# Kernel optimization log

Hardware: AMD Instinct MI355X
Metric: run time of the kernel (lower is better)

## Reference

```python
import jax, jax.numpy as jnp
import numpy as np
from jax import lax

N_QUBITS = 10
N_LAYERS = 6
DIM = 1 << N_QUBITS
EPS = 1e-5

_i = np.arange(DIM)
# Z_SIGNS[w, i] = (+1/-1) eigenvalue of PauliZ on wire w (wire 0 = most significant bit)
Z_SIGNS = jnp.asarray(np.stack([1.0 - 2.0 * ((_i >> (N_QUBITS - 1 - w)) & 1) for w in range(N_QUBITS)]).astype(np.float32))

def _layer_perm(r):
    # composed permutation of the ring of CNOT(w, (w+r)%n) gates of one StronglyEntanglingLayers layer
    p = _i.copy()
    for w in range(N_QUBITS):
        c, t = w, (w + r) % N_QUBITS
        pc, pt = N_QUBITS - 1 - c, N_QUBITS - 1 - t
        pg = _i ^ (((_i >> pc) & 1) << pt)
        p = p[pg]
    return p

LAYER_PERMS = [jnp.asarray(_layer_perm(l % (N_QUBITS - 1) + 1), dtype=jnp.int32) for l in range(N_LAYERS)]

def _apply_1q(state, U, wire):
    # state: (B, DIM) complex64; U: (2,2) or batched (B,2,2)
    B = state.shape[0]
    left = 1 << wire
    right = DIM // (2 * left)
    s = state.reshape(B, left, 2, right)
    if U.ndim == 3:
        out = jnp.einsum('bij,bljr->blir', U, s)
    else:
        out = jnp.einsum('ij,bljr->blir', U, s)
    return out.reshape(B, DIM)

def _ry_batched(theta):
    c = jnp.cos(theta / 2)
    s = jnp.sin(theta / 2)
    return jnp.stack([jnp.stack([c, -s], -1), jnp.stack([s, c], -1)], -2).astype(jnp.complex64)

def _rot(phi, theta, omega):
    # PennyLane Rot(phi, theta, omega) = RZ(omega) @ RY(theta) @ RZ(phi)
    c = jnp.cos(theta / 2)
    s = jnp.sin(theta / 2)
    m00 = jnp.exp(-1j * (phi + omega) / 2) * c
    m01 = -jnp.exp(1j * (phi - omega) / 2) * s
    m10 = jnp.exp(-1j * (phi - omega) / 2) * s
    m11 = jnp.exp(1j * (phi + omega) / 2) * c
    return jnp.stack([jnp.stack([m00, m01]), jnp.stack([m10, m11])]).astype(jnp.complex64)

def quantum_forward(xq, qw):
    # batched statevector simulation of: RY(pi*x_i) encoding + StronglyEntanglingLayers
    B = xq.shape[0]
    state = jnp.zeros((B, DIM), jnp.complex64).at[:, 0].set(1.0)
    for w in range(N_QUBITS):
        state = _apply_1q(state, _ry_batched(jnp.pi * xq[:, w]), w)
    for l in range(N_LAYERS):
        for w in range(N_QUBITS):
            state = _apply_1q(state, _rot(qw[l, w, 0], qw[l, w, 1], qw[l, w, 2]), w)
        state = state[:, LAYER_PERMS[l]]
    probs = state.real ** 2 + state.imag ** 2
    return probs @ Z_SIGNS.T  # (B, N_QUBITS) expvals of PauliZ

def _conv(x, w, b):
    y = lax.conv_general_dilated(x, w, (1, 1), 'SAME', dimension_numbers=('NCHW', 'OIHW', 'NCHW'))
    return y + b[None, :, None, None]

def _bn(x, g, b):
    # BatchNorm2d in training mode: per-batch statistics over (N, H, W)
    m = jnp.mean(x, (0, 2, 3), keepdims=True)
    v = jnp.var(x, (0, 2, 3), keepdims=True)
    return (x - m) * lax.rsqrt(v + EPS) * g[None, :, None, None] + b[None, :, None, None]

def _pool(x):
    return lax.reduce_window(x, -jnp.inf, lax.max, (1, 1, 2, 2), (1, 1, 2, 2), 'VALID')

def setup_inputs() -> dict:
    key = jax.random.key(0)
    ks = jax.random.split(key, 16)
    n = lambda k, sh, sc: jax.random.normal(k, sh, jnp.float32) * sc
    return {
        'x': jax.random.normal(ks[0], (256, 3, 64, 64), jnp.float32),
        'conv1_w': n(ks[1], (32, 3, 3, 3), 0.1), 'conv1_b': jnp.zeros(32),
        'bn1_g': jnp.ones(32), 'bn1_b': jnp.zeros(32),
        'conv2_w': n(ks[2], (32, 32, 3, 3), 0.05), 'conv2_b': jnp.zeros(32),
        'bn2_g': jnp.ones(32), 'bn2_b': jnp.zeros(32),
        'conv3_w': n(ks[3], (64, 32, 3, 3), 0.05), 'conv3_b': jnp.zeros(64),
        'bn3_g': jnp.ones(64), 'bn3_b': jnp.zeros(64),
        'conv4_w': n(ks[4], (64, 64, 3, 3), 0.05), 'conv4_b': jnp.zeros(64),
        'bn4_g': jnp.ones(64), 'bn4_b': jnp.zeros(64),
        'fc1_w': n(ks[5], (128, 64 * 16 * 16), 0.01), 'fc1_b': jnp.zeros(128),
        'fc2_w': n(ks[6], (10, 128), 0.05), 'fc2_b': jnp.zeros(10),
        'q_weights': jax.random.uniform(ks[7], (6, 10, 3), jnp.float32),
        'head_w': n(ks[8], (10, 10), 0.1), 'head_b': jnp.zeros(10),
    }

def reference(x, conv1_w, conv1_b, bn1_g, bn1_b, conv2_w, conv2_b, bn2_g, bn2_b,
              conv3_w, conv3_b, bn3_g, bn3_b, conv4_w, conv4_b, bn4_g, bn4_b,
              fc1_w, fc1_b, fc2_w, fc2_b, q_weights, head_w, head_b):
    h = jax.nn.relu(_bn(_conv(x, conv1_w, conv1_b), bn1_g, bn1_b))
    h = jax.nn.relu(_bn(_conv(h, conv2_w, conv2_b), bn2_g, bn2_b))
    h = _pool(h)  # Dropout(0.25) is identity in eval
    h = jax.nn.relu(_bn(_conv(h, conv3_w, conv3_b), bn3_g, bn3_b))
    h = jax.nn.relu(_bn(_conv(h, conv4_w, conv4_b), bn4_g, bn4_b))
    h = _pool(h)
    h = h.reshape(h.shape[0], -1)  # (B, 64*16*16)
    h = jax.nn.relu(h @ fc1_w.T + fc1_b)
    h = h @ fc2_w.T + fc2_b  # (B, n_qubits)
    q = quantum_forward(h, q_weights)
    return q @ head_w.T + head_b  # (B, num_classes)
```

## Files before the change

### kernel.cpp

```cpp
#include <hip/hip_runtime.h>
#include <math.h>

#define PI_F 3.14159265358979323846f

typedef __attribute__((ext_vector_type(8))) _Float16 half8;
typedef __attribute__((ext_vector_type(4))) _Float16 half4;
typedef __attribute__((ext_vector_type(4))) float f32x4;

__global__ __launch_bounds__(256) void prep_kernel(
    const float* __restrict__ x, _Float16* __restrict__ X4P,
    const float* __restrict__ w1, const float* __restrict__ w2,
    const float* __restrict__ w3, const float* __restrict__ w4,
    _Float16* __restrict__ t1, _Float16* __restrict__ t2,
    _Float16* __restrict__ t3, _Float16* __restrict__ t4,
    const float* __restrict__ f1w, _Float16* __restrict__ w1t,
    const float* __restrict__ qw, float* __restrict__ rotm,
    unsigned short* __restrict__ perm)
{
    const int b = blockIdx.x;
    const int t = threadIdx.x;
    if (b < 2380) {
        int pp = (b * 256 + t) * 2;
        half8 o;
        #pragma unroll
        for (int j = 0; j < 2; ++j) {
            int p = pp + j;
            int n = p / 4760;
            int rem = p - n * 4760;
            int yp = rem / 68, xp = rem - (rem / 68) * 68;
            int gy = yp - 2, gx = xp - 2;
            float v0 = 0.f, v1 = 0.f, v2 = 0.f;
            if (gy >= 0 && gy < 64 && gx >= 0 && gx < 64) {
                const float* xb = x + (size_t)n * 12288 + gy * 64 + gx;
                v0 = xb[0]; v1 = xb[4096]; v2 = xb[8192];
            }
            o[j * 4 + 0] = (_Float16)v0;
            o[j * 4 + 1] = (_Float16)v1;
            o[j * 4 + 2] = (_Float16)v2;
            o[j * 4 + 3] = (_Float16)0.f;
        }
        *(half8*)&X4P[(size_t)pp * 4] = o;
    } else if (b < 2640) {
        int idx = (b - 2380) * 256 + t;
        if (idx < 9216) {
            int j = idx & 7, co = (idx >> 3) & 31, k8 = idx >> 8;
            int k = k8 * 8 + j, tap = k >> 5, ci = k & 31;
            t2[idx] = (_Float16)w2[(size_t)(co * 32 + ci) * 9 + tap];
        } else if (idx < 27648) {
            int e = idx - 9216;
            int j = e & 7, co = (e >> 3) & 31, r = e >> 8;
            int k8 = r % 36, gg = r / 36;
            int k = k8 * 8 + j, tap = k >> 5, ci = k & 31;
            t3[e] = (_Float16)w3[(size_t)((gg * 32 + co) * 32 + ci) * 9 + tap];
        } else if (idx < 64512) {
            int e = idx - 27648;
            int j = e & 7, co = (e >> 3) & 31, r = e >> 8;
            int k8 = r % 36, gc = r / 36;
            int g = gc >> 1, cc = gc & 1;
            int kl = k8 * 8 + j, tap = kl >> 5, ci = cc * 32 + (kl & 31);
            t4[e] = (_Float16)w4[(size_t)((g * 32 + co) * 64 + ci) * 9 + tap];
        } else if (idx < 66560) {
            int e = idx - 64512;
            int j = e & 7, co = (e >> 3) & 31, k8 = e >> 8;
            int k = k8 * 8 + j, tap = k >> 2, ci = k & 3;
            t1[e] = (_Float16)((tap < 9 && ci < 3) ? w1[(size_t)(co * 3 + ci) * 9 + tap] : 0.f);
        }
    } else if (b < 3152) {
        __shared__ float lds[64][65];
        int b2 = b - 2640;
        const int yx0 = (b2 & 3) * 64;
        const int j = b2 >> 2;
        #pragma unroll
        for (int i = 0; i < 16; ++i) {
            int idx = t + 256 * i;
            int c = idx >> 6, yxl = idx & 63;
            lds[c][yxl] = f1w[(size_t)j * 16384 + c * 256 + yx0 + yxl];
        }
        __syncthreads();
        #pragma unroll
        for (int i = 0; i < 2; ++i) {
            int idx = t + 256 * i;
            int yxl = idx >> 3, c8 = idx & 7;
            half8 h;
            #pragma unroll
            for (int jj = 0; jj < 8; ++jj)
                h[jj] = (_Float16)lds[c8 * 8 + jj][yxl];
            *(half8*)&w1t[(size_t)j * 16384 + (size_t)(yx0 + yxl) * 64 + c8 * 8] = h;
        }
    } else {
        if (t < 60) {
            float phi = qw[t * 3], th = qw[t * 3 + 1], om = qw[t * 3 + 2];
            float c = cosf(0.5f * th), s = sinf(0.5f * th);
            float apo = 0.5f * (phi + om), amo = 0.5f * (phi - om);
            float cpo = cosf(apo), spo = sinf(apo);
            float cmo = cosf(amo), smo = sinf(amo);
            rotm[t * 8 + 0] = cpo * c;  rotm[t * 8 + 1] = -spo * c;
            rotm[t * 8 + 2] = -cmo * s; rotm[t * 8 + 3] = -smo * s;
            rotm[t * 8 + 4] = cmo * s;  rotm[t * 8 + 5] = -smo * s;
            rotm[t * 8 + 6] = cpo * c;  rotm[t * 8 + 7] = spo * c;
        }
        for (int e = t; e < 6144; e += 256) {
            int layer = e >> 10, i = e & 1023;
            int r = layer % 9 + 1;
            int jdx = i;
            for (int w = 9; w >= 0; --w) {
                int tt = (w + r) % 10;
                int pc = 9 - w, pt_ = 9 - tt;
                jdx ^= ((jdx >> pc) & 1) << pt_;
            }
            perm[e] = (unsigned short)jdx;
        }
    }
}

__global__ __launch_bounds__(256) void conv1_stats_kernel(
    const _Float16* __restrict__ X4P, const _Float16* __restrict__ w1m,
    const float* __restrict__ bias, float* __restrict__ partials)
{
    constexpr int TC = 66, TR = 6;
    constexpr int NPIX = (TR + 1) * TC;
    __shared__ __align__(16) _Float16 s_in[NPIX * 4];
    __shared__ __align__(16) _Float16 s_w[2048];
    __shared__ float s_red[64];

    const int t = threadIdx.x;
    const int row0 = blockIdx.x * 4;
    const int n = blockIdx.z;

    *(half8*)&s_w[t * 8] = *(const half8*)&w1m[t * 8];

    for (int p = t; p < NPIX; p += 256) {
        int col = p % TC, r = p / TC;
        uint2 u = make_uint2(0u, 0u);
        if (r < TR) {
            size_t pb = ((size_t)(n * 70 + row0 + r + 1) * 68 + col + 1) * 4;
            u = *(const uint2*)&X4P[pb];
        }
        *(uint2*)&s_in[p * 4] = u;
    }
    if (t < 64) s_red[t] = 0.f;
    __syncthreads();

    const int w = t >> 6, l = t & 63;
    const int lm = l & 15, lg = l >> 4;
    int pA[4];
    #pragma unroll
    for (int f = 0; f < 4; ++f) {
        int m = w * 64 + f * 16 + lm;
        pA[f] = (m >> 6) * TC + (m & 63);
    }
    f32x4 zero4 = {0.f, 0.f, 0.f, 0.f};
    f32x4 acc[4][2];
    #pragma unroll
    for (int f = 0; f < 4; ++f) { acc[f][0] = zero4; acc[f][1] = zero4; }

    {
        const int t0 = lg * 2;
        const int off0 = (t0 / 3) * TC + (t0 % 3);
        const int off1 = ((t0 + 1) / 3) * TC + ((t0 + 1) % 3);
        half8 b0 = *(const half8*)&s_w[(lg * 32 + lm) * 8];
        half8 b1 = *(const half8*)&s_w[(lg * 32 + 16 + lm) * 8];
        #pragma unroll
        for (int f = 0; f < 4; ++f) {
            half4 alo = *(const half4*)&s_in[(pA[f] + off0) * 4];
            half4 ahi = *(const half4*)&s_in[(pA[f] + off1) * 4];
            half8 a;
            #pragma unroll
            for (int j = 0; j < 4; ++j) { a[j] = alo[j]; a[4 + j] = ahi[j]; }
            acc[f][0] = __builtin_amdgcn_mfma_f32_16x16x32_f16(a, b0, acc[f][0], 0, 0, 0);
            acc[f][1] = __builtin_amdgcn_mfma_f32_16x16x32_f16(a, b1, acc[f][1], 0, 0, 0);
        }
    }
    {
        half8 b0 = *(const half8*)&s_w[((4 + lg) * 32 + lm) * 8];
        half8 b1 = *(const half8*)&s_w[((4 + lg) * 32 + 16 + lm) * 8];
        #pragma unroll
        for (int f = 0; f < 4; ++f) {
            half8 a;
            #pragma unroll
            for (int j = 0; j < 8; ++j) a[j] = (_Float16)0.f;
            if (lg == 0) {
                half4 alo = *(const half4*)&s_in[(pA[f] + 134) * 4];
                half4 ahi = *(const half4*)&s_in[(pA[f] + 198) * 4];
                #pragma unroll
                for (int j = 0; j < 4; ++j) { a[j] = alo[j]; a[4 + j] = ahi[j]; }
            }
            acc[f][0] = __builtin_amdgcn_mfma_f32_16x16x32_f16(a, b0, acc[f][0], 0, 0, 0);
            acc[f][1] = __builtin_amdgcn_mfma_f32_16x16x32_f16(a, b1, acc[f][1], 0, 0, 0);
        }
    }

    float bv0 = bias[lm];
    float bv1 = bias[16 + lm];
    float s0 = 0.f, s20 = 0.f, s1 = 0.f, s21 = 0.f;
    #pragma unroll
    for (int f = 0; f < 4; ++f) {
        #pragma unroll
        for (int r = 0; r < 4; ++r) {
            float v0 = acc[f][0][r] + bv0;
            float v1 = acc[f][1][r] + bv1;
            s0 += v0; s20 += v0 * v0;
            s1 += v1; s21 += v1 * v1;
        }
    }
    s0 += __shfl_xor(s0, 16);  s0 += __shfl_xor(s0, 32);
    s1 += __shfl_xor(s1, 16);  s1 += __shfl_xor(s1, 32);
    s20 += __shfl_xor(s20, 16); s20 += __shfl_xor(s20, 32);
    s21 += __shfl_xor(s21, 16); s21 += __shfl_xor(s21, 32);
    if (l < 16) {
        atomicAdd(&s_red[lm], s0);
        atomicAdd(&s_red[16 + lm], s1);
        atomicAdd(&s_red[32 + lm], s20);
        atomicAdd(&s_red[48 + lm], s21);
    }
    __syncthreads();
    if (t < 64)
        partials[((size_t)n * 16 + blockIdx.x) * 64 + t] = s_red[t];
}

__global__ __launch_bounds__(512, 6) void conv2_fused_kernel(
    const _Float16* __restrict__ X4P, const _Float16* __restrict__ w1m,
    const float* __restrict__ c1bias, const _Float16* __restrict__ ssh1,
    const _Float16* __restrict__ wt2, const float* __restrict__ c2bias,
    _Float16* __restrict__ out0, _Float16* __restrict__ out1,
    float* __restrict__ partials)
{
    constexpr int COUT = 32, MF = 4, NB = 2;
    constexpr int ROWS = 8;
    constexpr int TC = 66, NPIX = 10 * 66;
    constexpr int PS = 36;
    constexpr int XC = 68;
    __shared__ __align__(16) _Float16 s_in[NPIX * PS];
    __shared__ __align__(16) _Float16 s_w1[2048];
    __shared__ float s_red[64];

    const int t = threadIdx.x;
    const int row0 = blockIdx.x * ROWS;
    const int n = blockIdx.z;
    const int w = t >> 6, l = t & 63;
    const int lm = l & 15, lg = l >> 4;

    const _Float16* Xb = X4P + ((size_t)(n * 70 + row0) * 68) * 4;

    if (t < 256) *(half8*)&s_w1[t * 8] = *(const half8*)&w1m[t * 8];
    if (t < 64) s_red[t] = 0.f;
    __syncthreads();

    {
        const float b1v0 = c1bias[lm], b1v1 = c1bias[16 + lm];
        const _Float16 sc0 = ssh1[lm], sh0 = ssh1[32 + lm];
        const _Float16 sc1 = ssh1[16 + lm], sh1 = ssh1[48 + lm];
        for (int g = w; g < 42; g += 8) {
            int py = g * 16 + lm;
            int pyc = py < NPIX ? py : 0;
            int ry = pyc / 66, cy = pyc - ry * 66;
            int pb = ry * XC + cy;
            f32x4 a0 = {0.f, 0.f, 0.f, 0.f}, a1 = {0.f, 0.f, 0.f, 0.f};
            {
                const int t0 = lg * 2;
                const int off0 = (t0 / 3) * XC + (t0 % 3);
                const int off1 = ((t0 + 1) / 3) * XC + ((t0 + 1) % 3);
                half8 b0 = *(const half8*)&s_w1[(lg * 32 + lm) * 8];
                half8 b1 = *(const half8*)&s_w1[(lg * 32 + 16 + lm) * 8];
                half4 alo = *(const half4*)&Xb[(size_t)(pb + off0) * 4];
                half4 ahi = *(const half4*)&Xb[(size_t)(pb + off1) * 4];
                half8 a;
                #pragma unroll
                for (int j = 0; j < 4; ++j) { a[j] = alo[j]; a[4 + j] = ahi[j]; }
                a0 = __builtin_amdgcn_mfma_f32_16x16x32_f16(a, b0, a0, 0, 0, 0);
                a1 = __builtin_amdgcn_mfma_f32_16x16x32_f16(a, b1, a1, 0, 0, 0);
            }
            {
                half8 b0 = *(const half8*)&s_w1[((4 + lg) * 32 + lm) * 8];
                half8 b1 = *(const half8*)&s_w1[((4 + lg) * 32 + 16 + lm) * 8];
                half8 a;
                #pragma unroll
                for (int j = 0; j < 8; ++j) a[j] = (_Float16)0.f;
                if (lg == 0) {
                    half4 alo = *(const half4*)&Xb[(size_t)(pb + 138) * 4];
                    half4 ahi = *(const half4*)&Xb[(size_t)(pb + 204) * 4];
                    #pragma unroll
                    for (int j = 0; j < 4; ++j) { a[j] = alo[j]; a[4 + j] = ahi[j]; }
                }
                a0 = __builtin_amdgcn_mfma_f32_16x16x32_f16(a, b0, a0, 0, 0, 0);
                a1 = __builtin_amdgcn_mfma_f32_16x16x32_f16(a, b1, a1, 0, 0, 0);
            }
            #pragma unroll
            for (int r2 = 0; r2 < 4; ++r2) {
                int py2 = g * 16 + lg * 4 + r2;
                if (py2 < NPIX) {
                    int r2y = py2 / 66, c2y = py2 - r2y * 66;
                    int gy = row0 - 1 + r2y, gx = c2y - 1;
                    _Float16 y0 = (_Float16)0.f, y1 = (_Float16)0.f;
                    if (gy >= 0 && gy < 64 && gx >= 0 && gx < 64) {
                        _Float16 v0 = (_Float16)(a0[r2] + b1v0);
                        _Float16 v1 = (_Float16)(a1[r2] + b1v1);
                        _Float16 f0 = v0 * sc0 + sh0;
                        _Float16 f1 = v1 * sc1 + sh1;
                        y0 = f0 > (_Float16)0.f ? f0 : (_Float16)0.f;
                        y1 = f1 > (_Float16)0.f ? f1 : (_Float16)0.f;
                    }
                    s_in[py2 * PS + lm] = y0;
                    s_in[py2 * PS + 16 + lm] = y1;
                }
            }
        }
    }
    __syncthreads();

    int pA[MF];
    #pragma unroll
    for (int f = 0; f < MF; ++f)
        pA[f] = w * TC + f * 16 + lm;
    f32x4 zero4 = {0.f, 0.f, 0.f, 0.f};
    f32x4 acc[MF][NB];
    #pragma unroll
    for (int f = 0; f < MF; ++f)
        #pragma unroll
        for (int nb = 0; nb < NB; ++nb) acc[f][nb] = zero4;

    #pragma unroll
    for (int tap = 0; tap < 9; ++tap) {
        const int dy = tap / 3, dx = tap % 3;
        const int poff = dy * TC + dx;
        half8 b[NB];
        #pragma unroll
        for (int nb = 0; nb < NB; ++nb) {
            int col = nb * 16 + lm;
            b[nb] = *(const half8*)&wt2[((tap * 4 + lg) * 32 + col) * 8];
        }
        #pragma unroll
        for (int f = 0; f < MF; ++f) {
            int p = pA[f] + poff;
            half4 alo = *(const half4*)&s_in[p * PS + lg * 8];
            half4 ahi = *(const half4*)&s_in[p * PS + lg * 8 + 4];
            half8 a;
            #pragma unroll
            for (int j = 0; j < 4; ++j) { a[j] = alo[j]; a[4 + j] = ahi[j]; }
            #pragma unroll
            for (int nb = 0; nb < NB; ++nb)
                acc[f][nb] = __builtin_amdgcn_mfma_f32_16x16x32_f16(a, b[nb], acc[f][nb], 0, 0, 0);
        }
    }

    float bv[NB], s[NB], s2[NB];
    #pragma unroll
    for (int nb = 0; nb < NB; ++nb) {
        bv[nb] = c2bias[nb * 16 + lm];
        s[nb] = 0.f; s2[nb] = 0.f;
    }
    #pragma unroll
    for (int f = 0; f < MF; ++f) {
        #pragma unroll
        for (int nb = 0; nb < NB; ++nb) {
            #pragma unroll
            for (int r = 0; r < 4; ++r) {
                float v = acc[f][nb][r] + bv[nb];
                acc[f][nb][r] = v;
                s[nb] += v; s2[nb] += v * v;
            }
        }
    }
    #pragma unroll
    for (int nb = 0; nb < NB; ++nb) {
        s[nb] += __shfl_xor(s[nb], 16);  s[nb] += __shfl_xor(s[nb], 32);
        s2[nb] += __shfl_xor(s2[nb], 16); s2[nb] += __shfl_xor(s2[nb], 32);
    }
    if (l < 16) {
        #pragma unroll
        for (int nb = 0; nb < NB; ++nb) {
            atomicAdd(&s_red[nb * 16 + lm], s[nb]);
            atomicAdd(&s_red[32 + nb * 16 + lm], s2[nb]);
        }
    }

    {
        __syncthreads();
        _Float16* pk = s_in;
        #pragma unroll
        for (int nb = 0; nb < NB; ++nb) {
            #pragma unroll
            for (int f = 0; f < MF; ++f) {
                float v0 = acc[f][nb][0], v1 = acc[f][nb][1];
                float v2 = acc[f][nb][2], v3 = acc[f][nb][3];
                int xp0 = f * 8 + lg * 2;
                int o0 = (w * 32 + xp0) * COUT + nb * 16 + lm;
                int o1 = (w * 32 + xp0 + 1) * COUT + nb * 16 + lm;
                pk[o0] = (_Float16)fminf(v0, v1);
                pk[8192 + o0] = (_Float16)fmaxf(v0, v1);
                pk[o1] = (_Float16)fminf(v2, v3);
                pk[8192 + o1] = (_Float16)fmaxf(v2, v3);
            }
        }
        __syncthreads();
        int hp_row = t >> 7, rem = t & 127;
        int xp = rem >> 2, c8 = rem & 3;
        half8 mnA = *(const half8*)&pk[((2 * hp_row) * 32 + xp) * COUT + c8 * 8];
        half8 mnB = *(const half8*)&pk[((2 * hp_row + 1) * 32 + xp) * COUT + c8 * 8];
        half8 mxA = *(const half8*)&pk[8192 + ((2 * hp_row) * 32 + xp) * COUT + c8 * 8];
        half8 mxB = *(const half8*)&pk[8192 + ((2 * hp_row + 1) * 32 + xp) * COUT + c8 * 8];
        half8 mn, mx;
        #pragma unroll
        for (int j = 0; j < 8; ++j) {
            mn[j] = mnA[j] < mnB[j] ? mnA[j] : mnB[j];
            mx[j] = mxA[j] > mxB[j] ? mxA[j] : mxB[j];
        }
        size_t ob = (((size_t)n * 32 + (row0 >> 1) + hp_row) * 32 + xp) * COUT + c8 * 8;
        *(half8*)&out0[ob] = mn;
        *(half8*)&out1[ob] = mx;
    }

    __syncthreads();
    if (t < 64) {
        size_t bid = (size_t)n * gridDim.x + blockIdx.x;
        partials[bid * 64 + t] = s_red[t];
    }
}

template<int BLOCK, int W, int CIN, int COUT, int MF, int NB,
         bool MMIN, bool POOL>
__global__ __launch_bounds__(BLOCK, (BLOCK == 512 ? 4 : 3)) void conv_mfma_kernel(
    const _Float16* __restrict__ in0, const _Float16* __restrict__ in1,
    const _Float16* __restrict__ coef, const _Float16* __restrict__ wt,
    const float* __restrict__ bias,
    _Float16* __restrict__ out0, _Float16* __restrict__ out1,
    float* __restrict__ partials)
{
    constexpr int H = W;
    constexpr int NWAVE = BLOCK / 64;
    constexpr int SPW = MF * 16;
    constexpr int ROWS = NWAVE * SPW / W;
    constexpr int TR = ROWS + 2;
    constexpr int TC = W + 2;
    constexpr int NPIX = TR * TC;
    constexpr int NCH = CIN / 32;
    constexpr int C8N = CIN / 8;
    constexpr int KC = 288;
    constexpr int COUTB = NB * 16;
    __shared__ __align__(16) _Float16 s_in[NPIX * CIN];
    __shared__ float s_red[2 * COUTB];

    const int t = threadIdx.x;
    const int row0 = blockIdx.x * ROWS;
    const int n = blockIdx.z;

    const int w = t >> 6, l = t & 63;
    const int lm = l & 15, lg = l >> 4;
    int pA[MF];
    #pragma unroll
    for (int f = 0; f < MF; ++f) {
        int m = w * SPW + f * 16 + lm;
        pA[f] = (m / W) * TC + (m % W);
    }
    f32x4 zero4 = {0.f, 0.f, 0.f, 0.f};
    f32x4 acc[MF][NB];
    #pragma unroll
    for (int f = 0; f < MF; ++f)
        #pragma unroll
        for (int nb = 0; nb < NB; ++nb) acc[f][nb] = zero4;
    if (t < 2 * COUTB) s_red[t] = 0.f;

    for (int idx = t; idx < NPIX * C8N; idx += BLOCK) {
        int c8 = idx % C8N;
        int p = idx / C8N;
        int col = p % TC, r = p / TC;
        int gy = row0 + r - 1, gx = col - 1;
        half8 v;
        #pragma unroll
        for (int j = 0; j < 8; ++j) v[j] = (_Float16)0.f;
        if (gy >= 0 && gy < H && gx >= 0 && gx < W) {
            size_t gidx = (((size_t)n * H + gy) * W + gx) * CIN + c8 * 8;
            if (MMIN) {
                half8 mn = *(const half8*)&in0[gidx];
                half8 mx = *(const half8*)&in1[gidx];
                half8 sa = *(const half8*)&coef[c8 * 8];
                half8 sb = *(const half8*)&coef[CIN + c8 * 8];
                half8 sh = *(const half8*)&coef[2 * CIN + c8 * 8];
                #pragma unroll
                for (int j = 0; j < 8; ++j) {
                    _Float16 f = mx[j] * sa[j] + mn[j] * sb[j] + sh[j];
                    v[j] = f > (_Float16)0.f ? f : (_Float16)0.f;
                }
            } else {
                v = *(const half8*)&in0[gidx];
                if (coef) {
                    half8 sc = *(const half8*)&coef[c8 * 8];
                    half8 sh = *(const half8*)&coef[CIN + c8 * 8];
                    #pragma unroll
                    for (int j = 0; j < 8; ++j) {
                        _Float16 f = v[j] * sc[j] + sh[j];
                        v[j] = f > (_Float16)0.f ? f : (_Float16)0.f;
                    }
                }
            }
        }
        *(half8*)&s_in[(c8 * NPIX + p) * 8] = v;
    }
    __syncthreads();

    #pragma unroll
    for (int tap = 0; tap < 9; ++tap) {
        const int dy = tap / 3, dx = tap % 3;
        const int poff = dy * TC + dx;
        #pragma unroll
        for (int cc = 0; cc < NCH; ++cc) {
            half8 b[NB];
            #pragma unroll
            for (int nb = 0; nb < NB; ++nb) {
                int cog = nb * 16 + lm;
                int gg = cog >> 5, col = cog & 31;
                const _Float16* wp = wt + (size_t)(gg * NCH + cc) * KC * 32;
                b[nb] = *(const half8*)&wp[((tap * 4 + lg) * 32 + col) * 8];
            }
            #pragma unroll
            for (int f = 0; f < MF; ++f) {
                half8 a = *(const half8*)&s_in[((cc * 4 + lg) * NPIX + pA[f] + poff) * 8];
                #pragma unroll
                for (int nb = 0; nb < NB; ++nb)
                    acc[f][nb] = __builtin_amdgcn_mfma_f32_16x16x32_f16(a, b[nb], acc[f][nb], 0, 0, 0);
            }
        }
    }

    float bv[NB], s[NB], s2[NB];
    #pragma unroll
    for (int nb = 0; nb < NB; ++nb) {
        bv[nb] = bias[nb * 16 + lm];
        s[nb] = 0.f; s2[nb] = 0.f;
    }
    #pragma unroll
    for (int f = 0; f < MF; ++f) {
        #pragma unroll
        for (int r = 0; r < 4; ++r) {
            int m = w * SPW + f * 16 + lg * 4 + r;
            int yy = row0 + m / W, xo = m % W;
            size_t base = (((size_t)n * H + yy) * W + xo) * COUT;
            #pragma unroll
            for (int nb = 0; nb < NB; ++nb) {
                float v = acc[f][nb][r] + bv[nb];
                if (!POOL) out0[base + nb * 16 + lm] = (_Float16)v;
                s[nb] += v; s2[nb] += v * v;
            }
        }
    }
    #pragma unroll
    for (int nb = 0; nb < NB; ++nb) {
        s[nb] += __shfl_xor(s[nb], 16);  s[nb] += __shfl_xor(s[nb], 32);
        s2[nb] += __shfl_xor(s2[nb], 16); s2[nb] += __shfl_xor(s2[nb], 32);
    }
    if (l < 16) {
        #pragma unroll
        for (int nb = 0; nb < NB; ++nb) {
            atomicAdd(&s_red[nb * 16 + lm], s[nb]);
            atomicAdd(&s_red[COUTB + nb * 16 + lm], s2[nb]);
        }
    }

    if (POOL) {
        constexpr int FH = MF / 2;
        constexpr int PPIX = (ROWS / 2) * (W / 2);
        static_assert(2 * PPIX * COUT <= NPIX * CIN, "pool pack fits in s_in");
        __syncthreads();
        _Float16* pk = s_in;
        #pragma unroll
        for (int nb = 0; nb < NB; ++nb) {
            #pragma unroll
            for (int f = 0; f < FH; ++f) {
                #pragma unroll
                for (int rp = 0; rp < 2; ++rp) {
                    float a0 = acc[f][nb][2 * rp] + bv[nb];
                    float a1 = acc[f][nb][2 * rp + 1] + bv[nb];
                    float a2 = acc[f + FH][nb][2 * rp] + bv[nb];
                    float a3 = acc[f + FH][nb][2 * rp + 1] + bv[nb];
                    float mn = fminf(fminf(a0, a1), fminf(a2, a3));
                    float mx = fmaxf(fmaxf(a0, a1), fmaxf(a2, a3));
                    int xp = f * 8 + lg * 2 + rp;
                    int o = (w * (W / 2) + xp) * COUT + nb * 16 + lm;
                    pk[o] = (_Float16)mn;
                    pk[PPIX * COUT + o] = (_Float16)mx;
                }
            }
        }
        __syncthreads();
        size_t gb = (((size_t)n * (H / 2) + (row0 >> 1)) * (W / 2)) * COUT;
        for (int idx = t; idx < PPIX * COUT / 8; idx += BLOCK) {
            *(half8*)&out0[gb + (size_t)idx * 8] = *(const half8*)&pk[idx * 8];
            *(half8*)&out1[gb + (size_t)idx * 8] = *(const half8*)&pk[(PPIX * COUT + idx * 8)];
        }
    }

    __syncthreads();
    if (t < 2 * COUTB) {
        size_t bid = (size_t)n * gridDim.x + blockIdx.x;
        partials[bid * 2 * COUTB + t] = s_red[t];
    }
}

__global__ __launch_bounds__(256) void bn_finalize_kernel(
    const float* __restrict__ partials, int nx, float inv_count,
    const float* __restrict__ gamma, const float* __restrict__ beta,
    float* __restrict__ ss, _Float16* __restrict__ ssh,
    _Float16* __restrict__ sab, int COUT)
{
    const int c = blockIdx.x;
    const int t = threadIdx.x;
    float sum = 0.f, sq = 0.f;
    int total = 256 * nx;
    for (int e = t; e < total; e += 256) {
        size_t off = (size_t)e * 2 * COUT;
        sum += partials[off + c];
        sq  += partials[off + COUT + c];
    }
    #pragma unroll
    for (int off = 32; off > 0; off >>= 1) {
        sum += __shfl_xor(sum, off);
        sq  += __shfl_xor(sq, off);
    }
    __shared__ float rs[4], rq[4];
    if ((t & 63) == 0) { rs[t >> 6] = sum; rq[t >> 6] = sq; }
    __syncthreads();
    if (t == 0) {
        sum = rs[0] + rs[1] + rs[2] + rs[3];
        sq  = rq[0] + rq[1] + rq[2] + rq[3];
        float mean = sum * inv_count;
        float var = sq * inv_count - mean * mean;
        float scale = gamma[c] * rsqrtf(var + 1e-5f);
        float shift = beta[c] - mean * scale;
        ss[c] = scale;
        ss[COUT + c] = shift;
        if (ssh) {
            ssh[c] = (_Float16)scale;
            ssh[COUT + c] = (_Float16)shift;
        }
        if (sab) {
            sab[c] = (_Float16)(scale > 0.f ? scale : 0.f);
            sab[COUT + c] = (_Float16)(scale > 0.f ? 0.f : scale);
            sab[2 * COUT + c] = (_Float16)shift;
        }
    }
}

__global__ __launch_bounds__(256) void fc1_mfma_kernel(
    const _Float16* __restrict__ Amin, const _Float16* __restrict__ Amax,
    const _Float16* __restrict__ sab, const _Float16* __restrict__ Bw,
    float* __restrict__ hp)
{
    __shared__ __align__(16) _Float16 As[64][72];
    __shared__ __align__(16) _Float16 Bs[128][72];
    const int t = threadIdx.x;
    const int mt = blockIdx.x;
    const int kc = blockIdx.y;
    const int w = t >> 6, l = t & 63;
    const int lm = l & 15, lg = l >> 4;

    f32x4 zero4 = {0.f, 0.f, 0.f, 0.f};
    f32x4 acc[8];
    #pragma unroll
    for (int nb = 0; nb < 8; ++nb) acc[nb] = zero4;

    const size_t a_base = (size_t)(mt * 64) * 16384 + (size_t)kc * 512;
    const size_t b_base = (size_t)kc * 512;

    for (int p = 0; p < 8; ++p) {
        __syncthreads();
        #pragma unroll
        for (int i = 0; i < 2; ++i) {
            int idx = t + 256 * i;
            int r = idx >> 3, c8 = idx & 7;
            size_t off = a_base + (size_t)r * 16384 + p * 64 + c8 * 8;
            half8 mn = *(const half8*)&Amin[off];
            half8 mx = *(const half8*)&Amax[off];
            half8 sa = *(const half8*)&sab[c8 * 8];
            half8 sb = *(const half8*)&sab[64 + c8 * 8];
            half8 sh = *(const half8*)&sab[128 + c8 * 8];
            half8 v;
            #pragma unroll
            for (int j = 0; j < 8; ++j) {
                _Float16 f = mx[j] * sa[j] + mn[j] * sb[j] + sh[j];
                v[j] = f > (_Float16)0.f ? f : (_Float16)0.f;
            }
            *(half8*)&As[r][c8 * 8] = v;
        }
        #pragma unroll
        for (int i = 0; i < 4; ++i) {
            int idx = t + 256 * i;
            int r = idx >> 3, c8 = idx & 7;
            *(half8*)&Bs[r][c8 * 8] =
                *(const half8*)&Bw[b_base + (size_t)r * 16384 + p * 64 + c8 * 8];
        }
        __syncthreads();
        #pragma unroll
        for (int ks = 0; ks < 64; ks += 32) {
            half8 a = *(const half8*)&As[w * 16 + lm][ks + lg * 8];
            #pragma unroll
            for (int nb = 0; nb < 8; ++nb) {
                half8 b = *(const half8*)&Bs[nb * 16 + lm][ks + lg * 8];
                acc[nb] = __builtin_amdgcn_mfma_f32_16x16x32_f16(a, b, acc[nb], 0, 0, 0);
            }
        }
    }
    #pragma unroll
    for (int nb = 0; nb < 8; ++nb) {
        #pragma unroll
        for (int r = 0; r < 4; ++r) {
            int row = mt * 64 + w * 16 + lg * 4 + r;
            hp[((size_t)kc * 256 + row) * 128 + nb * 16 + lm] = acc[nb][r];
        }
    }
}

__global__ __launch_bounds__(128) void fcq_kernel(
    const float* __restrict__ hp, const float* __restrict__ f1b,
    const float* __restrict__ f2w, const float* __restrict__ f2b,
    const float* __restrict__ rotm, const unsigned short* __restrict__ perm,
    const float* __restrict__ head_w, const float* __restrict__ head_b,
    float* __restrict__ outp)
{
    __shared__ float lds[2048];
    __shared__ float hl[128];
    __shared__ float xql[10];
    const int n = blockIdx.x;
    const int t = threadIdx.x;

    {
        float s = f1b[t];
        #pragma unroll
        for (int kc = 0; kc < 32; ++kc) s += hp[((size_t)kc * 256 + n) * 128 + t];
        hl[t] = fmaxf(0.f, s);
    }
    __syncthreads();
    if (t < 10) {
        float o = f2b[t];
        #pragma unroll 4
        for (int k = 0; k < 128; ++k) o += f2w[t * 128 + k] * hl[k];
        xql[t] = o;
    }
    __syncthreads();
    if (t >= 64) return;

    const int l = t;
    float ar[16], ai[16];
    #pragma unroll
    for (int r = 0; r < 16; ++r) { ar[r] = 0.f; ai[r] = 0.f; }
    if (l == 0) ar[0] = 1.f;

    #pragma unroll
    for (int w = 0; w < 10; ++w) {
        float th = 0.5f * PI_F * xql[w];
        float c = cosf(th), s = sinf(th);
        const int k = 9 - w;
        if (k >= 6) {
            const int b = k - 6;
            #pragma unroll
            for (int r = 0; r < 16; ++r) {
                if (!(r & (1 << b))) {
                    int r1 = r | (1 << b);
                    float a0 = ar[r], a1 = ar[r1];
                    ar[r]  = c * a0 - s * a1;
                    ar[r1] = s * a0 + c * a1;
                }
            }
        } else {
            float ss = ((l >> k) & 1) ? s : -s;
            #pragma unroll
            for (int r = 0; r < 16; ++r) {
                float p = __shfl_xor(ar[r], 1 << k);
                ar[r] = c * ar[r] + ss * p;
            }
        }
    }

    #pragma unroll 1
    for (int layer = 0; layer < 6; ++layer) {
        #pragma unroll
        for (int w = 0; w < 10; ++w) {
            const float* m = rotm + (layer * 10 + w) * 8;
            float m00r = m[0], m00i = m[1], m01r = m[2], m01i = m[3];
            float m10r = m[4], m10i = m[5], m11r = m[6], m11i = m[7];
            const int k = 9 - w;
            if (k >= 6) {
                const int b = k - 6;
                #pragma unroll
                for (int r = 0; r < 16; ++r) {
                    if (!(r & (1 << b))) {
                        int r1 = r | (1 << b);
                        float a0r = ar[r], a0i = ai[r];
                        float a1r = ar[r1], a1i = ai[r1];
                        ar[r]  = m00r * a0r - m00i * a0i + m01r * a1r - m01i * a1i;
                        ai[r]  = m00r * a0i + m00i * a0r + m01r * a1i + m01i * a1r;
                        ar[r1] = m10r * a0r - m10i * a0i + m11r * a1r - m11i * a1i;
                        ai[r1] = m10r * a0i + m10i * a0r + m11r * a1i + m11i * a1r;
                    }
                }
            } else {
                int bit = (l >> k) & 1;
                float mAr = bit ? m11r : m00r, mAi = bit ? m11i : m00i;
                float mBr = bit ? m10r : m01r, mBi = bit ? m10i : m01i;
                #pragma unroll
                for (int r = 0; r < 16; ++r) {
                    float pr = __shfl_xor(ar[r], 1 << k);
                    float pi = __shfl_xor(ai[r], 1 << k);
                    float mr = ar[r], mi = ai[r];
                    ar[r] = mAr * mr - mAi * mi + mBr * pr - mBi * pi;
                    ai[r] = mAr * mi + mAi * mr + mBr * pi + mBi * pr;
                }
            }
        }
        #pragma unroll
        for (int r = 0; r < 16; ++r) {
            lds[(r << 6) | l] = ar[r];
            lds[1024 + ((r << 6) | l)] = ai[r];
        }
        __syncthreads();
        const unsigned short* pt = perm + layer * 1024;
        #pragma unroll
        for (int r = 0; r < 16; ++r) {
            int ji = pt[(r << 6) | l];
            ar[r] = lds[ji];
            ai[r] = lds[1024 + ji];
        }
        __syncthreads();
    }

    float S = 0.f, T0 = 0.f, T1 = 0.f, T2 = 0.f, T3 = 0.f;
    #pragma unroll
    for (int r = 0; r < 16; ++r) {
        float pr = ar[r] * ar[r] + ai[r] * ai[r];
        S += pr;
        T0 += (r & 1) ? -pr : pr;
        T1 += (r & 2) ? -pr : pr;
        T2 += (r & 4) ? -pr : pr;
        T3 += (r & 8) ? -pr : pr;
    }
    float pk[10];
    pk[0] = T3; pk[1] = T2; pk[2] = T1; pk[3] = T0;
    #pragma unroll
    for (int w = 4; w < 10; ++w)
        pk[w] = ((l >> (9 - w)) & 1) ? -S : S;
    #pragma unroll
    for (int w = 0; w < 10; ++w) {
        #pragma unroll
        for (int off = 1; off < 64; off <<= 1)
            pk[w] += __shfl_xor(pk[w], off);
    }
    if (l < 10) {
        float o = head_b[l];
        #pragma unroll
        for (int kk = 0; kk < 10; ++kk) o += pk[kk] * head_w[l * 10 + kk];
        outp[n * 10 + l] = o;
    }
}

extern "C" void kernel_launch(void* const* d_in, const int* in_sizes, int n_in,
                              void* d_out, int out_size, void* d_ws, size_t ws_size,
                              hipStream_t stream)
{
    const float* x   = (const float*)d_in[0];
    const float* c1w = (const float*)d_in[1];  const float* c1b = (const float*)d_in[2];
    const float* g1  = (const float*)d_in[3];  const float* b1  = (const float*)d_in[4];
    const float* c2w = (const float*)d_in[5];  const float* c2b = (const float*)d_in[6];
    const float* g2  = (const float*)d_in[7];  const float* b2  = (const float*)d_in[8];
    const float* c3w = (const float*)d_in[9];  const float* c3b = (const float*)d_in[10];
    const float* g3  = (const float*)d_in[11]; const float* b3  = (const float*)d_in[12];
    const float* c4w = (const float*)d_in[13]; const float* c4b = (const float*)d_in[14];
    const float* g4  = (const float*)d_in[15]; const float* b4  = (const float*)d_in[16];
    const float* f1w = (const float*)d_in[17]; const float* f1b = (const float*)d_in[18];
    const float* f2w = (const float*)d_in[19]; const float* f2b = (const float*)d_in[20];
    const float* qw  = (const float*)d_in[21];
    const float* hw  = (const float*)d_in[22]; const float* hb  = (const float*)d_in[23];

    float* ws = (float*)d_ws;
    _Float16* H0 = (_Float16*)ws;
    _Float16* H1 = H0 + 33554432;
    float* part = ws + 33554432;
    float* ss1  = part + 524288;
    float* ss2  = ss1 + 64;
    float* ss3  = ss2 + 64;
    float* ss4  = ss3 + 128;
    float* hp   = ss4 + 128;
    float* rotm = hp + 1048576;
    unsigned short* perm16 = (unsigned short*)(rotm + 480);
    _Float16* ssh1 = (_Float16*)(perm16 + 6144);
    _Float16* ssh3 = ssh1 + 64;
    _Float16* sab2 = ssh3 + 128;
    _Float16* sab4 = sab2 + 96;
    _Float16* wt2  = sab4 + 192;
    _Float16* wt3  = wt2 + 9216;
    _Float16* wt4  = wt3 + 18432;
    _Float16* w1m  = wt4 + 36864;
    _Float16* w1t  = w1m + 2048;
    _Float16* X4P  = w1t + 2097152;

    _Float16* minT2 = H1;
    _Float16* maxT2 = H1 + 8388608;
    _Float16* minT4 = H1;
    _Float16* maxT4 = H1 + 4194304;

    prep_kernel<<<3153, 256, 0, stream>>>(x, X4P, c1w, c2w, c3w, c4w,
                                          w1m, wt2, wt3, wt4, f1w, w1t,
                                          qw, rotm, perm16);

    conv1_stats_kernel<<<dim3(16, 1, 256), 256, 0, stream>>>(X4P, w1m, c1b, part);
    bn_finalize_kernel<<<32, 256, 0, stream>>>(part, 16, 1.f / 1048576.f,
                                               g1, b1, ss1, ssh1, nullptr, 32);

    conv2_fused_kernel<<<dim3(8, 1, 256), 512, 0, stream>>>(
        X4P, w1m, c1b, ssh1, wt2, c2b, minT2, maxT2, part);
    bn_finalize_kernel<<<32, 256, 0, stream>>>(part, 8, 1.f / 1048576.f,
                                               g2, b2, ss2, nullptr, sab2, 32);

    conv_mfma_kernel<512, 32, 32, 64, 4, 4, true, false>
        <<<dim3(2, 1, 256), 512, 0, stream>>>(
        minT2, maxT2, sab2, wt3, c3b, H0, nullptr, part);
    bn_finalize_kernel<<<64, 256, 0, stream>>>(part, 2, 1.f / 262144.f,
                                               g3, b3, ss3, ssh3, nullptr, 64);

    conv_mfma_kernel<512, 32, 64, 64, 4, 4, false, true>
        <<<dim3(2, 1, 256), 512, 0, stream>>>(
        H0, nullptr, ssh3, wt4, c4b, minT4, maxT4, part);
    bn_finalize_kernel<<<64, 256, 0, stream>>>(part, 2, 1.f / 262144.f,
                                               g4, b4, ss4, nullptr, sab4, 64);

    fc1_mfma_kernel<<<dim3(4, 32), 256, 0, stream>>>(minT4, maxT4, sab4, w1t, hp);

    fcq_kernel<<<256, 128, 0, stream>>>(hp, f1b, f2w, f2b,
                                        rotm, perm16, hw, hb, (float*)d_out);
}
```

Measured before the change: 194.0 us.

## Materialize conv1 output in fp16 instead of recomputing it inside conv2

```diff
diff --git a/kernel.cpp b/kernel.cpp
--- a/kernel.cpp
+++ b/kernel.cpp
@@ -115,12 +115,14 @@
 
 __global__ __launch_bounds__(256) void conv1_stats_kernel(
     const _Float16* __restrict__ X4P, const _Float16* __restrict__ w1m,
-    const float* __restrict__ bias, float* __restrict__ partials)
+    const float* __restrict__ bias, _Float16* __restrict__ Yg,
+    float* __restrict__ partials)
 {
     constexpr int TC = 66, TR = 6;
     constexpr int NPIX = (TR + 1) * TC;
     __shared__ __align__(16) _Float16 s_in[NPIX * 4];
     __shared__ __align__(16) _Float16 s_w[2048];
+    __shared__ __align__(16) _Float16 s_y[256 * 32];
     __shared__ float s_red[64];
 
     const int t = threadIdx.x;
@@ -199,6 +201,9 @@
         for (int r = 0; r < 4; ++r) {
             float v0 = acc[f][0][r] + bv0;
             float v1 = acc[f][1][r] + bv1;
+            int p_loc = w * 64 + f * 16 + lg * 4 + r;
+            s_y[p_loc * 32 + lm] = (_Float16)v0;
+            s_y[p_loc * 32 + 16 + lm] = (_Float16)v1;
             s0 += v0; s20 += v0 * v0;
             s1 += v1; s21 += v1 * v1;
         }
@@ -214,13 +219,21 @@
         atomicAdd(&s_red[48 + lm], s21);
     }
     __syncthreads();
+
+    {
+        _Float16* Yb = Yg + ((size_t)(n * 64 + row0) * 64) * 32;
+        #pragma unroll
+        for (int i = 0; i < 4; ++i) {
+            int idx = t + 256 * i;
+            *(half8*)&Yb[(size_t)idx * 8] = *(const half8*)&s_y[idx * 8];
+        }
+    }
     if (t < 64)
         partials[((size_t)n * 16 + blockIdx.x) * 64 + t] = s_red[t];
 }
 
 __global__ __launch_bounds__(512, 6) void conv2_fused_kernel(
-    const _Float16* __restrict__ X4P, const _Float16* __restrict__ w1m,
-    const float* __restrict__ c1bias, const _Float16* __restrict__ ssh1,
+    const _Float16* __restrict__ Yg, const _Float16* __restrict__ ssh1,
     const _Float16* __restrict__ wt2, const float* __restrict__ c2bias,
     _Float16* __restrict__ out0, _Float16* __restrict__ out1,
     float* __restrict__ partials)
@@ -229,9 +242,7 @@
     constexpr int ROWS = 8;
     constexpr int TC = 66, NPIX = 10 * 66;
     constexpr int PS = 36;
-    constexpr int XC = 68;
     __shared__ __align__(16) _Float16 s_in[NPIX * PS];
-    __shared__ __align__(16) _Float16 s_w1[2048];
     __shared__ float s_red[64];
 
     const int t = threadIdx.x;
@@ -240,70 +251,30 @@
     const int w = t >> 6, l = t & 63;
     const int lm = l & 15, lg = l >> 4;
 
-    const _Float16* Xb = X4P + ((size_t)(n * 70 + row0) * 68) * 4;
-
-    if (t < 256) *(half8*)&s_w1[t * 8] = *(const half8*)&w1m[t * 8];
     if (t < 64) s_red[t] = 0.f;
-    __syncthreads();
 
     {
-        const float b1v0 = c1bias[lm], b1v1 = c1bias[16 + lm];
-        const _Float16 sc0 = ssh1[lm], sh0 = ssh1[32 + lm];
-        const _Float16 sc1 = ssh1[16 + lm], sh1 = ssh1[48 + lm];
-        for (int g = w; g < 42; g += 8) {
-            int py = g * 16 + lm;
-            int pyc = py < NPIX ? py : 0;
-            int ry = pyc / 66, cy = pyc - ry * 66;
-            int pb = ry * XC + cy;
-            f32x4 a0 = {0.f, 0.f, 0.f, 0.f}, a1 = {0.f, 0.f, 0.f, 0.f};
-            {
-                const int t0 = lg * 2;
-                const int off0 = (t0 / 3) * XC + (t0 % 3);
-                const int off1 = ((t0 + 1) / 3) * XC + ((t0 + 1) % 3);
-                half8 b0 = *(const half8*)&s_w1[(lg * 32 + lm) * 8];
-                half8 b1 = *(const half8*)&s_w1[(lg * 32 + 16 + lm) * 8];
-                half4 alo = *(const half4*)&Xb[(size_t)(pb + off0) * 4];
-                half4 ahi = *(const half4*)&Xb[(size_t)(pb + off1) * 4];
-                half8 a;
+        const int c8 = t & 3;
+        half8 sc = *(const half8*)&ssh1[c8 * 8];
+        half8 sh = *(const half8*)&ssh1[32 + c8 * 8];
+        for (int idx = t; idx < NPIX * 4; idx += 512) {
+            int p = idx >> 2;
+            int py = p / 66, px = p - py * 66;
+            int gy = row0 - 1 + py, gx = px - 1;
+            half8 v;
+            #pragma unroll
+            for (int j = 0; j < 8; ++j) v[j] = (_Float16)0.f;
+            if (gy >= 0 && gy < 64 && gx >= 0 && gx < 64) {
+                half8 y = *(const half8*)&Yg[(((size_t)n * 64 + gy) * 64 + gx) * 32 + c8 * 8];
                 #pragma unroll
-                for (int j = 0; j < 4; ++j) { a[j] = alo[j]; a[4 + j] = ahi[j]; }
-                a0 = __builtin_amdgcn_mfma_f32_16x16x32_f16(a, b0, a0, 0, 0, 0);
-                a1 = __builtin_amdgcn_mfma_f32_16x16x32_f16(a, b1, a1, 0, 0, 0);
-            }
-            {
-                half8 b0 = *(const half8*)&s_w1[((4 + lg) * 32 + lm) * 8];
-                half8 b1 = *(const half8*)&s_w1[((4 + lg) * 32 + 16 + lm) * 8];
-                half8 a;
-                #pragma unroll
-                for (int j = 0; j < 8; ++j) a[j] = (_Float16)0.f;
-                if (lg == 0) {
-                    half4 alo = *(const half4*)&Xb[(size_t)(pb + 138) * 4];
-                    half4 ahi = *(const half4*)&Xb[(size_t)(pb + 204) * 4];
-                    #pragma unroll
-                    for (int j = 0; j < 4; ++j) { a[j] = alo[j]; a[4 + j] = ahi[j]; }
+                for (int j = 0; j < 8; ++j) {
+                    _Float16 f = y[j] * sc[j] + sh[j];
+                    v[j] = f > (_Float16)0.f ? f : (_Float16)0.f;
                 }
-                a0 = __builtin_amdgcn_mfma_f32_16x16x32_f16(a, b0, a0, 0, 0, 0);
-                a1 = __builtin_amdgcn_mfma_f32_16x16x32_f16(a, b1, a1, 0, 0, 0);
-            }
-            #pragma unroll
-            for (int r2 = 0; r2 < 4; ++r2) {
-                int py2 = g * 16 + lg * 4 + r2;
-                if (py2 < NPIX) {
-                    int r2y = py2 / 66, c2y = py2 - r2y * 66;
-                    int gy = row0 - 1 + r2y, gx = c2y - 1;
-                    _Float16 y0 = (_Float16)0.f, y1 = (_Float16)0.f;
-                    if (gy >= 0 && gy < 64 && gx >= 0 && gx < 64) {
-                        _Float16 v0 = (_Float16)(a0[r2] + b1v0);
-                        _Float16 v1 = (_Float16)(a1[r2] + b1v1);
-                        _Float16 f0 = v0 * sc0 + sh0;
-                        _Float16 f1 = v1 * sc1 + sh1;
-                        y0 = f0 > (_Float16)0.f ? f0 : (_Float16)0.f;
-                        y1 = f1 > (_Float16)0.f ? f1 : (_Float16)0.f;
-                    }
-                    s_in[py2 * PS + lm] = y0;
-                    s_in[py2 * PS + 16 + lm] = y1;
-                }
-            }
+            }
+            half4* vp = (half4*)&v;
+            *(half4*)&s_in[p * PS + c8 * 8] = vp[0];
+            *(half4*)&s_in[p * PS + c8 * 8 + 4] = vp[1];
         }
     }
     __syncthreads();
@@ -891,6 +862,7 @@
     _Float16* w1t  = w1m + 2048;
     _Float16* X4P  = w1t + 2097152;
 
+    _Float16* Yg    = H0;
     _Float16* minT2 = H1;
     _Float16* maxT2 = H1 + 8388608;
     _Float16* minT4 = H1;
@@ -900,12 +872,13 @@
                                           w1m, wt2, wt3, wt4, f1w, w1t,
                                           qw, rotm, perm16);
 
-    conv1_stats_kernel<<<dim3(16, 1, 256), 256, 0, stream>>>(X4P, w1m, c1b, part);
+    conv1_stats_kernel<<<dim3(16, 1, 256), 256, 0, stream>>>(
+        X4P, w1m, c1b, Yg, part);
     bn_finalize_kernel<<<32, 256, 0, stream>>>(part, 16, 1.f / 1048576.f,
                                                g1, b1, ss1, ssh1, nullptr, 32);
 
     conv2_fused_kernel<<<dim3(8, 1, 256), 512, 0, stream>>>(
-        X4P, w1m, c1b, ssh1, wt2, c2b, minT2, maxT2, part);
+        Yg, ssh1, wt2, c2b, minT2, maxT2, part);
     bn_finalize_kernel<<<32, 256, 0, stream>>>(part, 8, 1.f / 1048576.f,
                                                g2, b2, ss2, nullptr, sab2, 32);
 
```

Result: no change. 194.9 us (+0.4%).
